# Kernel optimization log

Measured on AMD Instinct MI355X. Metric: run time of the kernel, lower is better.

## Reference

```python
import jax, jax.numpy as jnp
import numpy as np

B, N, F_IN, F_OUT = 1, 8192, 256, 256
ALPHA = 0.2  # leaky relu negative slope
NEG_INF = -9e15


def setup_inputs() -> dict:
    key = jax.random.key(0)
    ks = jax.random.split(key, 8)
    feat = jax.random.normal(ks[0], (B, N, F_IN), dtype=jnp.float32)
    adj = jax.random.randint(ks[1], (B, N, N), 0, 2, dtype=jnp.int32)
    s = 1.414 * (6.0 / (F_IN + F_OUT)) ** 0.5
    W = jax.random.uniform(ks[2], (F_IN, F_OUT), minval=-s, maxval=s, dtype=jnp.float32)
    a_1 = jax.random.normal(ks[3], (F_OUT, 1), dtype=jnp.float32) * 0.1
    a_2 = jax.random.normal(ks[4], (F_OUT, 1), dtype=jnp.float32) * 0.1
    a_12 = jax.random.normal(ks[5], (F_OUT, F_OUT), dtype=jnp.float32) * (1.0 / F_OUT ** 0.5)
    W_1 = jax.random.uniform(ks[6], (F_IN, F_OUT), minval=-s, maxval=s, dtype=jnp.float32)
    W_2 = jax.random.uniform(ks[7], (F_IN, F_OUT), minval=-s, maxval=s, dtype=jnp.float32)
    return {"feat": feat, "adj": adj, "W": W, "a_1": a_1, "a_2": a_2,
            "a_12": a_12, "W_1": W_1, "W_2": W_2}


def reference(feat, adj, W, a_1, a_2, a_12, W_1, W_2):
    # --- attention logits ---
    h = jnp.matmul(feat, W)                       # [B,N,D]
    Ax = jnp.matmul(h, a_1)                       # [B,N,1]
    Ay = jnp.matmul(h, a_2)                       # [B,N,1]
    A_xy = jnp.matmul(jnp.matmul(h, a_12), jnp.swapaxes(h, 1, 2))  # [B,N,N]
    logits = jnp.swapaxes(Ax, 1, 2) + Ay + A_xy   # Ax^T broadcast over rows
    e = jax.nn.leaky_relu(logits, negative_slope=ALPHA)
    e = jnp.where(adj > 0, e, NEG_INF)
    attention = jax.nn.softmax(e, axis=-1)        # dropout is no-op (eval)
    # --- aggregate over RAW features ---
    h_prime = jnp.matmul(attention, feat)         # [B,N,F_IN]
    # --- dual linear update ---
    h_out = jnp.matmul(feat, W_1) + jnp.matmul(h_prime, W_2)
    return jax.nn.elu(h_out)
```

## Files before the change

kernel.cpp:

```cpp
#include <hip/hip_runtime.h>


typedef __attribute__((ext_vector_type(8))) _Float16 f16x8;
typedef __attribute__((ext_vector_type(4))) float f32x4;

#define NN 8192
#define DD 256
#define NSPLIT 2
#define NPART 2
#define CHUNK (NN / NSPLIT)
#define KVB 64
#define BM 32
#define NT (CHUNK / KVB)

#define MFMA16(a, b, c) __builtin_amdgcn_mfma_f32_16x16x32_f16(a, b, c, 0, 0, 0)
#define BAR_LGKM() asm volatile("s_waitcnt lgkmcnt(0)\n\ts_barrier" ::: "memory")
#define BAR_VM() asm volatile("s_waitcnt vmcnt(0)\n\ts_barrier" ::: "memory")

__device__ __forceinline__ short f2h(float f) {
  union { _Float16 h; short s; } u; u.h = (_Float16)f; return u.s;
}
__device__ __forceinline__ float h2f(short b) {
  union { short s; _Float16 h; } u; u.s = b; return (float)u.h;
}

typedef __attribute__((address_space(3))) unsigned lds_u32;
typedef const __attribute__((address_space(1))) unsigned glb_u32;
__device__ __forceinline__ void gl2lds16(const void* g, void* l) {
  __builtin_amdgcn_global_load_lds((glb_u32*)g, (lds_u32*)l, 16, 0, 0);
}

__global__ __launch_bounds__(256) void cvt_split_kernel(const float* __restrict__ in,
                                                        short* __restrict__ hi,
                                                        short* __restrict__ lo, int n) {
  for (int i = blockIdx.x * blockDim.x + threadIdx.x; i < n; i += gridDim.x * blockDim.x) {
    float f = in[i];
    short h = f2h(f);
    hi[i] = h;
    lo[i] = f2h(f - h2f(h));
  }
}

__global__ __launch_bounds__(256) void featT_kernel(const float* __restrict__ feat,
                                                    short* __restrict__ fT) {
  __shared__ float tile[32][33];
  const int i0 = blockIdx.x * 32, c0 = blockIdx.y * 32;
  const int r = threadIdx.x >> 5, c = threadIdx.x & 31;
#pragma unroll
  for (int p = 0; p < 4; ++p)
    tile[p * 8 + r][c] = feat[(size_t)(i0 + p * 8 + r) * DD + c0 + c];
  __syncthreads();
#pragma unroll
  for (int p = 0; p < 4; ++p)
    fT[(size_t)(c0 + p * 8 + r) * NN + i0 + c] = f2h(tile[c][p * 8 + r]);
}

__global__ __launch_bounds__(256) void transpose_split_kernel(const float* __restrict__ in,
                                                              short* __restrict__ tHi,
                                                              short* __restrict__ tLo) {
  int r = blockIdx.x, c = threadIdx.x;
  float f = in[r * DD + c];
  short h = f2h(f);
  tHi[c * DD + r] = h;
  if (tLo) tLo[c * DD + r] = f2h(f - h2f(h));
}

__global__ __launch_bounds__(256) void gemm_kernel(
    const short* __restrict__ Ahi, const short* __restrict__ Alo,
    const short* __restrict__ BThi, const short* __restrict__ BTlo,
    const short* __restrict__ A2, const short* __restrict__ BT2,
    short* __restrict__ outH, float* __restrict__ outF, int doElu) {
  const int lane = threadIdx.x & 63;
  const int w = threadIdx.x >> 6;
  const int l15 = lane & 15;
  const int koff = (lane >> 4) * 8;
  const int row0 = blockIdx.x * 64 + w * 16;
  const int col0 = blockIdx.y * 64;
  f32x4 acc[4] = {};
  const int aoff = (row0 + l15) * DD + koff;
#pragma unroll
  for (int kk = 0; kk < 8; ++kk) {
    f16x8 ah = *(const f16x8*)(Ahi + aoff + kk * 32);
#pragma unroll
    for (int cf = 0; cf < 4; ++cf) {
      int boff = (col0 + cf * 16 + l15) * DD + kk * 32 + koff;
      f16x8 bh = *(const f16x8*)(BThi + boff);
      acc[cf] = MFMA16(ah, bh, acc[cf]);
      if (Alo) {
        f16x8 al = *(const f16x8*)(Alo + aoff + kk * 32);
        acc[cf] = MFMA16(al, bh, acc[cf]);
      }
      if (BTlo) {
        f16x8 bl = *(const f16x8*)(BTlo + boff);
        acc[cf] = MFMA16(ah, bl, acc[cf]);
      }
    }
  }
  if (A2) {
#pragma unroll
    for (int kk = 0; kk < 8; ++kk) {
      f16x8 ah = *(const f16x8*)(A2 + aoff + kk * 32);
#pragma unroll
      for (int cf = 0; cf < 4; ++cf) {
        f16x8 bh = *(const f16x8*)(BT2 + (col0 + cf * 16 + l15) * DD + kk * 32 + koff);
        acc[cf] = MFMA16(ah, bh, acc[cf]);
      }
    }
  }
  const int crow = row0 + (lane >> 4) * 4;
#pragma unroll
  for (int cf = 0; cf < 4; ++cf) {
    int col = col0 + cf * 16 + l15;
#pragma unroll
    for (int r = 0; r < 4; ++r) {
      float v = acc[cf][r];
      if (doElu) v = (v > 0.f) ? v : expm1f(v);
      if (outF) outF[(crow + r) * DD + col] = v;
      if (outH) outH[(crow + r) * DD + col] = f2h(v);
    }
  }
}

__global__ __launch_bounds__(256) void axay_kernel(const short* __restrict__ hF,
                                                   const float* __restrict__ a1,
                                                   const float* __restrict__ a2,
                                                   float* __restrict__ ax,
                                                   float* __restrict__ ay) {
  const int lane = threadIdx.x & 63;
  const int w = threadIdx.x >> 6;
  const int row = blockIdx.x * 4 + w;
  float s1 = 0.f, s2 = 0.f;
#pragma unroll
  for (int j = 0; j < 4; ++j) {
    int k = lane * 4 + j;
    float hv = h2f(hF[row * DD + k]);
    s1 += hv * a1[k];
    s2 += hv * a2[k];
  }
#pragma unroll
  for (int m = 1; m < 64; m <<= 1) {
    s1 += __shfl_xor(s1, m);
    s2 += __shfl_xor(s2, m);
  }
  if (lane == 0) { ax[row] = s1; ay[row] = s2; }
}

__global__ __launch_bounds__(256, 2) void attn_kernel(
    const short* __restrict__ gF, const short* __restrict__ hF,
    const short* __restrict__ fT, const float* __restrict__ ax,
    const float* __restrict__ ay, const int* __restrict__ adj,
    short* __restrict__ numPart, float* __restrict__ mPart,
    float* __restrict__ lPart) {
  __shared__ short sG[BM * DD];
  __shared__ short sH[KVB * DD];
  __shared__ float sS[BM][68];
  __shared__ short sP[BM][72];
  __shared__ float sScale[BM];

  const int tid = threadIdx.x;
  const int lane = tid & 63;
  const int w = tid >> 6;
  const int wr = w >> 1, sp = w & 1;
  const int l15 = lane & 15;
  const int q0 = lane >> 4;
  const int crow = q0 * 4;

  const int bid = blockIdx.x;
  const int chunk = (bid & 7) >> 2;
  const int rowblk = (bid >> 3) * 4 + (bid & 3);
  const int row0 = rowblk * BM;
  const int jbase = chunk * CHUNK;

  float ay4[4];
#pragma unroll
  for (int r = 0; r < 4; ++r) ay4[r] = ay[row0 + wr * 16 + crow + r];

#pragma unroll
  for (int R = 0; R < 4; ++R) {
    int dstb = R * 4096 + tid * 16;
    int lr = dstb >> 9;
    int srcb = (dstb & 511) ^ ((lr & 7) << 4);
    gl2lds16(gF + (row0 + lr) * DD + (srcb >> 1), (char*)sG + dstb);
  }
  auto stageH = [&](int jrow) {
#pragma unroll
    for (int R = 0; R < 8; ++R) {
      int dstb = R * 4096 + tid * 16;
      int lr = dstb >> 9;
      int srcb = (dstb & 511) ^ ((lr & 7) << 4);
      gl2lds16(hF + (jrow + lr) * DD + (srcb >> 1), (char*)sH + dstb);
    }
  };
  stageH(jbase);

  const size_t adjrow = (size_t)(row0 + wr * 16 + crow) * NN;
  int a8[2][4];
  float ax2[2];
#pragma unroll
  for (int cf = 0; cf < 2; ++cf) {
    int kb = jbase + sp * 32 + cf * 16 + l15;
    ax2[cf] = ax[kb];
#pragma unroll
    for (int r = 0; r < 4; ++r)
      a8[cf][r] = __builtin_nontemporal_load(adj + adjrow + (size_t)r * NN + kb);
  }

  const int srow = tid >> 3;
  const int sc8 = (tid & 7) * 8;
  float m_run = -__builtin_inff();
  float l_run = 0.f;
  f32x4 accpv[2][4] = {};

  BAR_VM();

  for (int t = 0; t < NT; ++t) {
    const int j0 = jbase + t * KVB;
    f32x4 aA = {}, aB = {};
    {
      const int lrA = wr * 16 + l15;
      const int rbA = lrA * 512, swzA = (lrA & 7) << 4;
      const int lrB0 = sp * 32 + l15;
      const int rbB0 = lrB0 * 512, swzB0 = (lrB0 & 7) << 4;
      const int lrB1 = sp * 32 + 16 + l15;
      const int rbB1 = lrB1 * 512, swzB1 = (lrB1 & 7) << 4;
      __builtin_amdgcn_s_setprio(1);
#pragma unroll
      for (int kk = 0; kk < 8; ++kk) {
        const int slot = kk * 64 + q0 * 16;
        f16x8 ga = *(const f16x8*)((const char*)sG + rbA + (slot ^ swzA));
        f16x8 b0 = *(const f16x8*)((const char*)sH + rbB0 + (slot ^ swzB0));
        f16x8 b1 = *(const f16x8*)((const char*)sH + rbB1 + (slot ^ swzB1));
        aA = MFMA16(ga, b0, aA);
        aB = MFMA16(ga, b1, aB);
      }
      __builtin_amdgcn_s_setprio(0);
    }
#pragma unroll
    for (int cf = 0; cf < 2; ++cf) {
      const f32x4& ac = cf ? aB : aA;
#pragma unroll
      for (int r = 0; r < 4; ++r) {
        float v = ac[r] + ax2[cf] + ay4[r];
        v = (v > 0.f) ? v : 0.2f * v;
        sS[wr * 16 + crow + r][sp * 32 + cf * 16 + l15] =
            (a8[cf][r] > 0) ? v : -9.0e15f;
      }
    }
    BAR_LGKM();
    f16x8 vb[2][4];
#pragma unroll
    for (int ks = 0; ks < 2; ++ks)
#pragma unroll
      for (int df = 0; df < 4; ++df)
        vb[ks][df] = *(const f16x8*)(fT + (size_t)(w * 64 + df * 16 + l15) * NN +
                                     j0 + ks * 32 + q0 * 8);
    int a8n[2][4];
    float ax2n[2];
    {
      int jn = (t + 1 < NT) ? (j0 + KVB) : jbase;
#pragma unroll
      for (int cf = 0; cf < 2; ++cf) {
        int kb = jn + sp * 32 + cf * 16 + l15;
        ax2n[cf] = ax[kb];
#pragma unroll
        for (int r = 0; r < 4; ++r)
          a8n[cf][r] = __builtin_nontemporal_load(adj + adjrow + (size_t)r * NN + kb);
      }
    }
    if (t + 1 < NT) stageH(j0 + KVB);
    {
      float4 s0 = *(const float4*)(&sS[srow][sc8]);
      float4 s1 = *(const float4*)(&sS[srow][sc8 + 4]);
      float tmax = fmaxf(fmaxf(fmaxf(s0.x, s0.y), fmaxf(s0.z, s0.w)),
                         fmaxf(fmaxf(s1.x, s1.y), fmaxf(s1.z, s1.w)));
      tmax = fmaxf(tmax, __shfl_xor(tmax, 1));
      tmax = fmaxf(tmax, __shfl_xor(tmax, 2));
      tmax = fmaxf(tmax, __shfl_xor(tmax, 4));
      float m_new = fmaxf(m_run, tmax);
      float scale = __expf(m_run - m_new);
      float p[8];
      p[0] = __expf(s0.x - m_new); p[1] = __expf(s0.y - m_new);
      p[2] = __expf(s0.z - m_new); p[3] = __expf(s0.w - m_new);
      p[4] = __expf(s1.x - m_new); p[5] = __expf(s1.y - m_new);
      p[6] = __expf(s1.z - m_new); p[7] = __expf(s1.w - m_new);
      float psum = ((p[0] + p[1]) + (p[2] + p[3])) + ((p[4] + p[5]) + (p[6] + p[7]));
      psum += __shfl_xor(psum, 1);
      psum += __shfl_xor(psum, 2);
      psum += __shfl_xor(psum, 4);
      l_run = l_run * scale + psum;
      m_run = m_new;
      union { short s[8]; f16x8 v; } pu;
#pragma unroll
      for (int c = 0; c < 8; ++c) pu.s[c] = f2h(p[c]);
      *(f16x8*)(&sP[srow][sc8]) = pu.v;
      if ((tid & 7) == 0) sScale[srow] = scale;
    }
    BAR_LGKM();
    {
      float4 sc0 = *(const float4*)(&sScale[crow]);
      float4 sc1 = *(const float4*)(&sScale[16 + crow]);
      const float* scp[2] = { &sc0.x, &sc1.x };
#pragma unroll
      for (int rg = 0; rg < 2; ++rg)
#pragma unroll
        for (int df = 0; df < 4; ++df)
#pragma unroll
          for (int r = 0; r < 4; ++r) accpv[rg][df][r] *= scp[rg][r];
      __builtin_amdgcn_s_setprio(1);
#pragma unroll
      for (int ks = 0; ks < 2; ++ks) {
        f16x8 pa0 = *(const f16x8*)(&sP[l15][ks * 32 + q0 * 8]);
        f16x8 pa1 = *(const f16x8*)(&sP[16 + l15][ks * 32 + q0 * 8]);
#pragma unroll
        for (int df = 0; df < 4; ++df) {
          accpv[0][df] = MFMA16(pa0, vb[ks][df], accpv[0][df]);
          accpv[1][df] = MFMA16(pa1, vb[ks][df], accpv[1][df]);
        }
      }
      __builtin_amdgcn_s_setprio(0);
    }
#pragma unroll
    for (int cf = 0; cf < 2; ++cf) {
#pragma unroll
      for (int r = 0; r < 4; ++r) a8[cf][r] = a8n[cf][r];
      ax2[cf] = ax2n[cf];
    }
    BAR_VM();
  }
  if ((tid & 7) == 0) {
    mPart[chunk * NN + row0 + srow] = m_run;
    lPart[chunk * NN + row0 + srow] = l_run;
  }
  short* np = numPart + (size_t)chunk * NN * DD;
#pragma unroll
  for (int rg = 0; rg < 2; ++rg)
#pragma unroll
    for (int df = 0; df < 4; ++df) {
      int col = w * 64 + df * 16 + l15;
#pragma unroll
      for (int r = 0; r < 4; ++r)
        np[(size_t)(row0 + rg * 16 + crow + r) * DD + col] = f2h(accpv[rg][df][r]);
    }
}

__global__ __launch_bounds__(256) void combine_kernel(
    const short* __restrict__ numPart, const float* __restrict__ mPart,
    const float* __restrict__ lPart, short* __restrict__ hp) {
  const int row = blockIdx.x;
  const int col = threadIdx.x;
  float m[NPART], l[NPART];
  float ms = -__builtin_inff();
#pragma unroll
  for (int i = 0; i < NPART; ++i) {
    m[i] = mPart[i * NN + row];
    l[i] = lPart[i * NN + row];
    ms = fmaxf(ms, m[i]);
  }
  float denom = 0.f, num = 0.f;
  const size_t idx = (size_t)row * DD + col;
#pragma unroll
  for (int i = 0; i < NPART; ++i) {
    float wgt = __expf(m[i] - ms);
    denom += l[i] * wgt;
    num += h2f(numPart[(size_t)i * NN * DD + idx]) * wgt;
  }
  hp[idx] = f2h(num / denom);
}

extern "C" void kernel_launch(void* const* d_in, const int* in_sizes, int n_in,
                              void* d_out, int out_size, void* d_ws, size_t ws_size,
                              hipStream_t stream) {
  const float* feat = (const float*)d_in[0];
  const int*   adj  = (const int*)d_in[1];
  const float* W    = (const float*)d_in[2];
  const float* a1   = (const float*)d_in[3];
  const float* a2   = (const float*)d_in[4];
  const float* a12  = (const float*)d_in[5];
  const float* W1   = (const float*)d_in[6];
  const float* W2   = (const float*)d_in[7];
  float* out = (float*)d_out;
  (void)in_sizes; (void)n_in; (void)out_size; (void)ws_size;

  char* ws = (char*)d_ws;
  size_t off = 0;
  auto alloc = [&](size_t b) { void* p = ws + off; off += (b + 255) & ~(size_t)255; return p; };
  short* featHi = (short*)alloc((size_t)NN * DD * 2);
  short* featLo = (short*)alloc((size_t)NN * DD * 2);
  short* fT     = (short*)alloc((size_t)NN * DD * 2);
  short* hF     = (short*)alloc((size_t)NN * DD * 2);
  short* gF     = (short*)alloc((size_t)NN * DD * 2);
  short* hp     = (short*)alloc((size_t)NN * DD * 2);
  short* WTh    = (short*)alloc((size_t)DD * DD * 2);
  short* WTl    = (short*)alloc((size_t)DD * DD * 2);
  short* A12Th  = (short*)alloc((size_t)DD * DD * 2);
  short* A12Tl  = (short*)alloc((size_t)DD * DD * 2);
  short* W1T    = (short*)alloc((size_t)DD * DD * 2);
  short* W2T    = (short*)alloc((size_t)DD * DD * 2);
  float* axv    = (float*)alloc((size_t)NN * 4);
  float* ayv    = (float*)alloc((size_t)NN * 4);
  short* numPart = (short*)alloc((size_t)NPART * NN * DD * 2);
  float* mPart   = (float*)alloc((size_t)NPART * NN * 4);
  float* lPart   = (float*)alloc((size_t)NPART * NN * 4);

  cvt_split_kernel<<<2048, 256, 0, stream>>>(feat, featHi, featLo, NN * DD);
  featT_kernel<<<dim3(NN / 32, DD / 32), 256, 0, stream>>>(feat, fT);
  transpose_split_kernel<<<DD, DD, 0, stream>>>(W, WTh, WTl);
  transpose_split_kernel<<<DD, DD, 0, stream>>>(a12, A12Th, A12Tl);
  transpose_split_kernel<<<DD, DD, 0, stream>>>(W1, W1T, nullptr);
  transpose_split_kernel<<<DD, DD, 0, stream>>>(W2, W2T, nullptr);
  gemm_kernel<<<dim3(NN / 64, DD / 64), 256, 0, stream>>>(
      featHi, featLo, WTh, WTl, nullptr, nullptr, hF, nullptr, 0);
  gemm_kernel<<<dim3(NN / 64, DD / 64), 256, 0, stream>>>(
      hF, nullptr, A12Th, A12Tl, nullptr, nullptr, gF, nullptr, 0);
  axay_kernel<<<NN / 4, 256, 0, stream>>>(hF, a1, a2, axv, ayv);
  attn_kernel<<<dim3((NN / BM) * NSPLIT), 256, 0, stream>>>(
      gF, hF, fT, axv, ayv, adj, numPart, mPart, lPart);
  combine_kernel<<<NN, DD, 0, stream>>>(numPart, mPart, lPart, hp);
  gemm_kernel<<<dim3(NN / 64, DD / 64), 256, 0, stream>>>(
      featHi, nullptr, W1T, nullptr, hp, W2T, nullptr, out, 1);
}
```

Measured before the change: 308.7 us.

## Compute softmax stats in registers, drop score LDS buffer, raise occupancy

```diff
diff --git a/kernel.cpp b/kernel.cpp
--- a/kernel.cpp
+++ b/kernel.cpp
@@ -145,7 +145,7 @@
   if (lane == 0) { ax[row] = s1; ay[row] = s2; }
 }
 
-__global__ __launch_bounds__(256, 2) void attn_kernel(
+__global__ __launch_bounds__(256, 3) void attn_kernel(
     const short* __restrict__ gF, const short* __restrict__ hF,
     const short* __restrict__ fT, const float* __restrict__ ax,
     const float* __restrict__ ay, const int* __restrict__ adj,
@@ -153,9 +153,10 @@
     float* __restrict__ lPart) {
   __shared__ short sG[BM * DD];
   __shared__ short sH[KVB * DD];
-  __shared__ float sS[BM][68];
   __shared__ short sP[BM][72];
-  __shared__ float sScale[BM];
+  __shared__ short sM[2][32];
+  __shared__ float sSum[2][32];
+  __shared__ float sScale[32];
 
   const int tid = threadIdx.x;
   const int lane = tid & 63;
@@ -170,10 +171,11 @@
   const int rowblk = (bid >> 3) * 4 + (bid & 3);
   const int row0 = rowblk * BM;
   const int jbase = chunk * CHUNK;
+  const int myrow = wr * 16 + crow;
 
   float ay4[4];
 #pragma unroll
-  for (int r = 0; r < 4; ++r) ay4[r] = ay[row0 + wr * 16 + crow + r];
+  for (int r = 0; r < 4; ++r) ay4[r] = ay[row0 + myrow + r];
 
 #pragma unroll
   for (int R = 0; R < 4; ++R) {
@@ -193,28 +195,26 @@
   };
   stageH(jbase);
 
-  const size_t adjrow = (size_t)(row0 + wr * 16 + crow) * NN;
-  int a8[2][4];
-  float ax2[2];
-#pragma unroll
-  for (int cf = 0; cf < 2; ++cf) {
-    int kb = jbase + sp * 32 + cf * 16 + l15;
-    ax2[cf] = ax[kb];
-#pragma unroll
-    for (int r = 0; r < 4; ++r)
-      a8[cf][r] = __builtin_nontemporal_load(adj + adjrow + (size_t)r * NN + kb);
-  }
-
-  const int srow = tid >> 3;
-  const int sc8 = (tid & 7) * 8;
-  float m_run = -__builtin_inff();
-  float l_run = 0.f;
+  const size_t adjrow = (size_t)(row0 + myrow) * NN;
+  float m_run[4], l_run[4];
+#pragma unroll
+  for (int r = 0; r < 4; ++r) { m_run[r] = -__builtin_inff(); l_run[r] = 0.f; }
   f32x4 accpv[2][4] = {};
 
   BAR_VM();
 
   for (int t = 0; t < NT; ++t) {
     const int j0 = jbase + t * KVB;
+    int a8[2][4];
+    float ax2[2];
+#pragma unroll
+    for (int cf = 0; cf < 2; ++cf) {
+      int kb = j0 + sp * 32 + cf * 16 + l15;
+      ax2[cf] = ax[kb];
+#pragma unroll
+      for (int r = 0; r < 4; ++r)
+        a8[cf][r] = __builtin_nontemporal_load(adj + adjrow + (size_t)r * NN + kb);
+    }
     f32x4 aA = {}, aB = {};
     {
       const int lrA = wr * 16 + l15;
@@ -235,6 +235,7 @@
       }
       __builtin_amdgcn_s_setprio(0);
     }
+    float s8[2][4];
 #pragma unroll
     for (int cf = 0; cf < 2; ++cf) {
       const f32x4& ac = cf ? aB : aA;
@@ -242,60 +243,63 @@
       for (int r = 0; r < 4; ++r) {
         float v = ac[r] + ax2[cf] + ay4[r];
         v = (v > 0.f) ? v : 0.2f * v;
-        sS[wr * 16 + crow + r][sp * 32 + cf * 16 + l15] =
-            (a8[cf][r] > 0) ? v : -9.0e15f;
-      }
+        s8[cf][r] = (a8[cf][r] > 0) ? v : -9.0e15f;
+      }
+    }
+    float tmax[4];
+#pragma unroll
+    for (int r = 0; r < 4; ++r) tmax[r] = fmaxf(s8[0][r], s8[1][r]);
+#pragma unroll
+    for (int msk = 1; msk < 16; msk <<= 1)
+#pragma unroll
+      for (int r = 0; r < 4; ++r)
+        tmax[r] = fmaxf(tmax[r], __shfl_xor(tmax[r], msk));
+#pragma unroll
+    for (int r = 0; r < 4; ++r) tmax[r] = fmaxf(tmax[r], -60000.f);
+    if (l15 == 0) {
+#pragma unroll
+      for (int r = 0; r < 4; ++r) sM[sp][myrow + r] = f2h(tmax[r]);
     }
     BAR_LGKM();
-    f16x8 vb[2][4];
-#pragma unroll
-    for (int ks = 0; ks < 2; ++ks)
-#pragma unroll
-      for (int df = 0; df < 4; ++df)
-        vb[ks][df] = *(const f16x8*)(fT + (size_t)(w * 64 + df * 16 + l15) * NN +
-                                     j0 + ks * 32 + q0 * 8);
-    int a8n[2][4];
-    float ax2n[2];
-    {
-      int jn = (t + 1 < NT) ? (j0 + KVB) : jbase;
-#pragma unroll
-      for (int cf = 0; cf < 2; ++cf) {
-        int kb = jn + sp * 32 + cf * 16 + l15;
-        ax2n[cf] = ax[kb];
-#pragma unroll
-        for (int r = 0; r < 4; ++r)
-          a8n[cf][r] = __builtin_nontemporal_load(adj + adjrow + (size_t)r * NN + kb);
-      }
-    }
     if (t + 1 < NT) stageH(j0 + KVB);
-    {
-      float4 s0 = *(const float4*)(&sS[srow][sc8]);
-      float4 s1 = *(const float4*)(&sS[srow][sc8 + 4]);
-      float tmax = fmaxf(fmaxf(fmaxf(s0.x, s0.y), fmaxf(s0.z, s0.w)),
-                         fmaxf(fmaxf(s1.x, s1.y), fmaxf(s1.z, s1.w)));
-      tmax = fmaxf(tmax, __shfl_xor(tmax, 1));
-      tmax = fmaxf(tmax, __shfl_xor(tmax, 2));
-      tmax = fmaxf(tmax, __shfl_xor(tmax, 4));
-      float m_new = fmaxf(m_run, tmax);
-      float scale = __expf(m_run - m_new);
-      float p[8];
-      p[0] = __expf(s0.x - m_new); p[1] = __expf(s0.y - m_new);
-      p[2] = __expf(s0.z - m_new); p[3] = __expf(s0.w - m_new);
-      p[4] = __expf(s1.x - m_new); p[5] = __expf(s1.y - m_new);
-      p[6] = __expf(s1.z - m_new); p[7] = __expf(s1.w - m_new);
-      float psum = ((p[0] + p[1]) + (p[2] + p[3])) + ((p[4] + p[5]) + (p[6] + p[7]));
-      psum += __shfl_xor(psum, 1);
-      psum += __shfl_xor(psum, 2);
-      psum += __shfl_xor(psum, 4);
-      l_run = l_run * scale + psum;
-      m_run = m_new;
-      union { short s[8]; f16x8 v; } pu;
-#pragma unroll
-      for (int c = 0; c < 8; ++c) pu.s[c] = f2h(p[c]);
-      *(f16x8*)(&sP[srow][sc8]) = pu.v;
-      if ((tid & 7) == 0) sScale[srow] = scale;
+    float scale[4], psum[4];
+#pragma unroll
+    for (int r = 0; r < 4; ++r) {
+      float om = h2f(sM[sp ^ 1][myrow + r]);
+      float m_new = fmaxf(m_run[r], fmaxf(tmax[r], om));
+      scale[r] = __expf(m_run[r] - m_new);
+      m_run[r] = m_new;
+    }
+#pragma unroll
+    for (int cf = 0; cf < 2; ++cf)
+#pragma unroll
+      for (int r = 0; r < 4; ++r) {
+        float p = __expf(s8[cf][r] - m_run[r]);
+        s8[cf][r] = p;
+      }
+#pragma unroll
+    for (int r = 0; r < 4; ++r) psum[r] = s8[0][r] + s8[1][r];
+#pragma unroll
+    for (int msk = 1; msk < 16; msk <<= 1)
+#pragma unroll
+      for (int r = 0; r < 4; ++r) psum[r] += __shfl_xor(psum[r], msk);
+#pragma unroll
+    for (int cf = 0; cf < 2; ++cf)
+#pragma unroll
+      for (int r = 0; r < 4; ++r)
+        sP[myrow + r][sp * 32 + cf * 16 + l15] = f2h(s8[cf][r]);
+    if (l15 == 0) {
+#pragma unroll
+      for (int r = 0; r < 4; ++r) sSum[sp][myrow + r] = psum[r];
+      if (sp == 0) {
+#pragma unroll
+        for (int r = 0; r < 4; ++r) sScale[myrow + r] = scale[r];
+      }
     }
     BAR_LGKM();
+#pragma unroll
+    for (int r = 0; r < 4; ++r)
+      l_run[r] = l_run[r] * scale[r] + psum[r] + sSum[sp ^ 1][myrow + r];
     {
       float4 sc0 = *(const float4*)(&sScale[crow]);
       float4 sc1 = *(const float4*)(&sScale[16 + crow]);
@@ -306,6 +310,15 @@
         for (int df = 0; df < 4; ++df)
 #pragma unroll
           for (int r = 0; r < 4; ++r) accpv[rg][df][r] *= scp[rg][r];
+    }
+    {
+      f16x8 vb[2][4];
+#pragma unroll
+      for (int ks = 0; ks < 2; ++ks)
+#pragma unroll
+        for (int df = 0; df < 4; ++df)
+          vb[ks][df] = *(const f16x8*)(fT + (size_t)(w * 64 + df * 16 + l15) * NN +
+                                       j0 + ks * 32 + q0 * 8);
       __builtin_amdgcn_s_setprio(1);
 #pragma unroll
       for (int ks = 0; ks < 2; ++ks) {
@@ -319,17 +332,14 @@
       }
       __builtin_amdgcn_s_setprio(0);
     }
-#pragma unroll
-    for (int cf = 0; cf < 2; ++cf) {
-#pragma unroll
-      for (int r = 0; r < 4; ++r) a8[cf][r] = a8n[cf][r];
-      ax2[cf] = ax2n[cf];
-    }
     BAR_VM();
   }
-  if ((tid & 7) == 0) {
-    mPart[chunk * NN + row0 + srow] = m_run;
-    lPart[chunk * NN + row0 + srow] = l_run;
+  if (sp == 0 && l15 == 0) {
+#pragma unroll
+    for (int r = 0; r < 4; ++r) {
+      mPart[chunk * NN + row0 + myrow + r] = m_run[r];
+      lPart[chunk * NN + row0 + myrow + r] = l_run[r];
+    }
   }
   short* np = numPart + (size_t)chunk * NN * DD;
 #pragma unroll
```

New measurement: 354.8 us. +14.9%, slower.
